# Performance work log

Measured on AMD Instinct MI355X. Metric: run time of the kernel, lower is better.

Reference implementation:

```python
import jax, jax.numpy as jnp
import numpy as np

B, R, N = 1, 1024, 128
C_FEAT, C_MSA, C_PAIR = 22, 256, 128
NBINS = 65  # relpos bins, vbins = arange(65) - 32


def setup_inputs() -> dict:
    key = jax.random.key(0)
    ks = jax.random.split(key, 9)
    w = lambda k, shape: (jax.random.normal(k, shape, jnp.float32) * 0.05)
    return {
        "target_feat": jax.random.normal(ks[0], (B, R, C_FEAT), jnp.float32),
        "residue_index": jnp.broadcast_to(jnp.arange(R, dtype=jnp.int32), (B, R)),
        "msa_feat": jax.random.normal(ks[1], (B, N, R, C_FEAT), jnp.float32),
        "Wa": w(ks[2], (C_PAIR, C_FEAT)), "ba": jnp.zeros((C_PAIR,), jnp.float32),
        "Wb": w(ks[3], (C_PAIR, C_FEAT)), "bb": jnp.zeros((C_PAIR,), jnp.float32),
        "Wm1": w(ks[4], (C_MSA, C_FEAT)), "bm1": jnp.zeros((C_MSA,), jnp.float32),
        "Wm2": w(ks[5], (C_MSA, C_FEAT)), "bm2": jnp.zeros((C_MSA,), jnp.float32),
        "Wpos": w(ks[6], (C_PAIR, NBINS)), "bpos": jnp.zeros((C_PAIR,), jnp.float32),
    }


def reference(target_feat, residue_index, msa_feat,
              Wa, ba, Wb, bb, Wm1, bm1, Wm2, bm2, Wpos, bpos):
    # pair init: z[b,i,j] = to_a(tf)[b,j] + to_b(tf)[b,i]
    a = target_feat @ Wa.T + ba                      # (b, r, c_pair)
    bv = target_feat @ Wb.T + bb                     # (b, r, c_pair)
    z = a[:, None, :, :] + bv[:, :, None, :]         # (b, r, r, c_pair)

    # relpos: nearest-bin one-hot of d = ri[j] - ri[i] against arange(65)-32,
    # then Linear(65 -> c_pair).  One-hot @ W.T is exactly an embedding gather
    # of row clip(d+32, 0, 64) from Wpos.T, so skip materializing the one-hot.
    d = residue_index[:, None, :] - residue_index[:, :, None]  # (b, r, r)
    bins = jnp.clip(d + (NBINS // 2), 0, NBINS - 1)            # (b, r, r) int
    z = z + Wpos.T[bins] + bpos                                # gather + bias

    # MSA init: m = to_m1(msa_feat) + to_m2(target_feat) broadcast over n rows
    m = (msa_feat @ Wm1.T + bm1) + (target_feat @ Wm2.T + bm2)[:, None, :, :]
    return m, z
```

## Files before the change

kernel.cpp:

```cpp
#include <hip/hip_runtime.h>

#define RR     1024
#define NSEQ   128
#define CFEAT  22
#define CMSA   256
#define CPAIR  128
#define NBINS  65

typedef float f4 __attribute__((ext_vector_type(4)));

__global__ __launch_bounds__(256) void k_pre(
    const float* __restrict__ tf,
    const float* __restrict__ Wa, const float* __restrict__ ba,
    const float* __restrict__ Wb, const float* __restrict__ bb,
    const float* __restrict__ Wm2, const float* __restrict__ bm2,
    const float* __restrict__ Wpos, const float* __restrict__ bpos,
    float* __restrict__ a, float* __restrict__ bvp,
    float* __restrict__ tm2, float* __restrict__ pose)
{
    __shared__ float wlds[CFEAT][512];
    __shared__ float row[CFEAT];
    const int r = blockIdx.x;
    const int t = threadIdx.x;

    for (int idx = t; idx < 128 * CFEAT; idx += 256) {
        int c = idx / CFEAT, k = idx - c * CFEAT;
        wlds[k][c] = Wa[idx];
    }
    for (int idx = t; idx < 128 * CFEAT; idx += 256) {
        int c = idx / CFEAT, k = idx - c * CFEAT;
        wlds[k][128 + c] = Wb[idx];
    }
    for (int idx = t; idx < 256 * CFEAT; idx += 256) {
        int c = idx / CFEAT, k = idx - c * CFEAT;
        wlds[k][256 + c] = Wm2[idx];
    }
    if (t < CFEAT) row[t] = tf[r * CFEAT + t];
    __syncthreads();

    float s1 = 0.f, s2 = 0.f;
    #pragma unroll
    for (int k = 0; k < CFEAT; ++k) {
        float rv = row[k];
        s1 += rv * wlds[k][t];
        s2 += rv * wlds[k][256 + t];
    }
    tm2[(long)r * CMSA + t] = s2 + bm2[t];
    if (t < CPAIR) a[(long)r * CPAIR + t] = s1 + ba[t];
    else           bvp[(long)r * CPAIR + (t - CPAIR)] = s1 + bb[t - CPAIR];

    if (r < NBINS && t < CPAIR)
        pose[r * CPAIR + t] = Wpos[t * NBINS + r] + bpos[t];
}

#define PPB 64
__global__ __launch_bounds__(256) void k_msa(
    const float* __restrict__ msa,
    const float* __restrict__ Wm1, const float* __restrict__ bm1,
    const float* __restrict__ tm2, float* __restrict__ out_m)
{
    __shared__ float wt[CFEAT][CMSA];
    __shared__ float rows[PPB][24];
    const int t = threadIdx.x;

    for (int idx = t; idx < CMSA * CFEAT; idx += 256) {
        int c = idx / CFEAT, k = idx - c * CFEAT;
        wt[k][c] = Wm1[idx];
    }
    const long pbase = (long)blockIdx.x * PPB;
    const float* src = msa + pbase * CFEAT;
    for (int idx = t; idx < PPB * CFEAT; idx += 256) {
        int p = idx / CFEAT, k = idx - p * CFEAT;
        rows[p][k] = src[idx];
    }
    if (t < PPB) { rows[t][22] = 0.f; rows[t][23] = 0.f; }
    __syncthreads();

    const int c  = (t & 63) * 4;
    const int wv = t >> 6;

    f4 wr[24];
    #pragma unroll
    for (int k = 0; k < CFEAT; ++k) wr[k] = *(const f4*)&wt[k][c];
    wr[22] = (f4){0.f, 0.f, 0.f, 0.f};
    wr[23] = (f4){0.f, 0.f, 0.f, 0.f};
    const f4 b4 = *(const f4*)(bm1 + c);

    for (int it = 0; it < PPB / 4; ++it) {
        const int p = it * 4 + wv;
        const long pair = pbase + p;
        const int r = (int)(pair & (RR - 1));
        f4 acc = (f4){0.f, 0.f, 0.f, 0.f};
        #pragma unroll
        for (int k4 = 0; k4 < 6; ++k4) {
            f4 mv = *(const f4*)&rows[p][k4 * 4];
            acc += mv.x * wr[k4 * 4 + 0];
            acc += mv.y * wr[k4 * 4 + 1];
            acc += mv.z * wr[k4 * 4 + 2];
            acc += mv.w * wr[k4 * 4 + 3];
        }
        const f4 t4 = *(const f4*)(tm2 + (long)r * CMSA + c);
        f4 o = acc + b4 + t4;
        __builtin_nontemporal_store(o, (f4*)(out_m + pair * CMSA + c));
    }
}

__global__ __launch_bounds__(256) void k_pair(
    const int* __restrict__ resi,
    const float* __restrict__ a, const float* __restrict__ bvp,
    const float* __restrict__ pose, float* __restrict__ out_z)
{
    const int bx = blockIdx.x;
    const int i = bx >> 4;
    const int jbase = (bx & 15) * 64;
    const int t = threadIdx.x;
    const int c4 = (t & 31);
    const int jo = t >> 5;

    const int ri = resi[i];
    const f4 bvv = *(const f4*)(bvp + (long)i * CPAIR + c4 * 4);

    #pragma unroll
    for (int jj = 0; jj < 64; jj += 8) {
        const int j = jbase + jj + jo;
        int d = resi[j] - ri + (NBINS / 2);
        d = min(max(d, 0), NBINS - 1);
        const f4 av = *(const f4*)(a + (long)j * CPAIR + c4 * 4);
        const f4 pv = *(const f4*)(pose + (long)d * CPAIR + c4 * 4);
        f4 o = av + bvv + pv;
        __builtin_nontemporal_store(
            o, (f4*)(out_z + ((long)i * RR + j) * CPAIR + c4 * 4));
    }
}

extern "C" void kernel_launch(void* const* d_in, const int* in_sizes, int n_in,
                              void* d_out, int out_size, void* d_ws, size_t ws_size,
                              hipStream_t stream) {
    const float* tf   = (const float*)d_in[0];
    const int*   resi = (const int*)  d_in[1];
    const float* msa  = (const float*)d_in[2];
    const float* Wa   = (const float*)d_in[3];
    const float* ba   = (const float*)d_in[4];
    const float* Wb   = (const float*)d_in[5];
    const float* bb   = (const float*)d_in[6];
    const float* Wm1  = (const float*)d_in[7];
    const float* bm1  = (const float*)d_in[8];
    const float* Wm2  = (const float*)d_in[9];
    const float* bm2  = (const float*)d_in[10];
    const float* Wpos = (const float*)d_in[11];
    const float* bpos = (const float*)d_in[12];

    float* out_m = (float*)d_out;
    float* out_z = out_m + (long)NSEQ * RR * CMSA;

    float* a    = (float*)d_ws;
    float* bvp  = a   + (long)RR * CPAIR;
    float* tm2  = bvp + (long)RR * CPAIR;
    float* pose = tm2 + (long)RR * CMSA;

    k_pre<<<RR, 256, 0, stream>>>(tf, Wa, ba, Wb, bb, Wm2, bm2, Wpos, bpos,
                                  a, bvp, tm2, pose);
    k_msa<<<(NSEQ * RR) / PPB, 256, 0, stream>>>(msa, Wm1, bm1, tm2, out_m);
    k_pair<<<RR * 16, 256, 0, stream>>>(resi, a, bvp, pose, out_z);
}
```

Before: 161.5 us.

## Batch rows per block in prep kernel and stage pose table in LDS for pair kernel

The prep kernel now handles 8 residues per block, so the LDS weight transpose is amortised over 8 rows instead of redone 1024 times. The pair kernel switches to one block per row i with 512 threads. Each block stages the 65x128 pose table and the residue indices in LDS, so the gather reads LDS instead of global memory. This cuts redundant weight loads and launch overhead, but each pair block pays about 37 KB of LDS staging, which may limit occupancy on what is mainly a store-bound kernel.

```diff
diff --git a/kernel.cpp b/kernel.cpp
--- a/kernel.cpp
+++ b/kernel.cpp
@@ -19,9 +19,9 @@
     float* __restrict__ tm2, float* __restrict__ pose)
 {
     __shared__ float wlds[CFEAT][512];
-    __shared__ float row[CFEAT];
-    const int r = blockIdx.x;
+    __shared__ float rows[8][CFEAT];
     const int t = threadIdx.x;
+    const int r0 = blockIdx.x * 8;
 
     for (int idx = t; idx < 128 * CFEAT; idx += 256) {
         int c = idx / CFEAT, k = idx - c * CFEAT;
@@ -35,22 +35,29 @@
         int c = idx / CFEAT, k = idx - c * CFEAT;
         wlds[k][256 + c] = Wm2[idx];
     }
-    if (t < CFEAT) row[t] = tf[r * CFEAT + t];
+    for (int idx = t; idx < 8 * CFEAT; idx += 256) {
+        int rr = idx / CFEAT, k = idx - rr * CFEAT;
+        rows[rr][k] = tf[(r0 + rr) * CFEAT + k];
+    }
     __syncthreads();
 
-    float s1 = 0.f, s2 = 0.f;
     #pragma unroll
-    for (int k = 0; k < CFEAT; ++k) {
-        float rv = row[k];
-        s1 += rv * wlds[k][t];
-        s2 += rv * wlds[k][256 + t];
+    for (int rr = 0; rr < 8; ++rr) {
+        const int r = r0 + rr;
+        float s1 = 0.f, s2 = 0.f;
+        #pragma unroll
+        for (int k = 0; k < CFEAT; ++k) {
+            float rv = rows[rr][k];
+            s1 += rv * wlds[k][t];
+            s2 += rv * wlds[k][256 + t];
+        }
+        tm2[r * CMSA + t] = s2 + bm2[t];
+        if (t < CPAIR) a[r * CPAIR + t] = s1 + ba[t];
+        else           bvp[r * CPAIR + (t - CPAIR)] = s1 + bb[t - CPAIR];
     }
-    tm2[(long)r * CMSA + t] = s2 + bm2[t];
-    if (t < CPAIR) a[(long)r * CPAIR + t] = s1 + ba[t];
-    else           bvp[(long)r * CPAIR + (t - CPAIR)] = s1 + bb[t - CPAIR];
 
-    if (r < NBINS && t < CPAIR)
-        pose[r * CPAIR + t] = Wpos[t * NBINS + r] + bpos[t];
+    if (blockIdx.x < NBINS && t < CPAIR)
+        pose[blockIdx.x * CPAIR + t] = Wpos[t * NBINS + blockIdx.x] + bpos[t];
 }
 
 #define PPB 64
@@ -105,31 +112,37 @@
     }
 }
 
-__global__ __launch_bounds__(256) void k_pair(
+__global__ __launch_bounds__(512) void k_pair(
     const int* __restrict__ resi,
     const float* __restrict__ a, const float* __restrict__ bvp,
     const float* __restrict__ pose, float* __restrict__ out_z)
 {
-    const int bx = blockIdx.x;
-    const int i = bx >> 4;
-    const int jbase = (bx & 15) * 64;
+    __shared__ float poseL[NBINS][CPAIR];
+    __shared__ int   rjL[RR];
+    const int i = blockIdx.x;
     const int t = threadIdx.x;
-    const int c4 = (t & 31);
+
+    for (int idx = t; idx < NBINS * CPAIR; idx += 512)
+        (&poseL[0][0])[idx] = pose[idx];
+    for (int idx = t; idx < RR; idx += 512)
+        rjL[idx] = resi[idx];
+    __syncthreads();
+
+    const int c4 = (t & 31) * 4;
     const int jo = t >> 5;
+    const int ri = rjL[i];
+    const f4 bvv = *(const f4*)(bvp + (long)i * CPAIR + c4);
+    float* dst = out_z + (long)i * RR * CPAIR;
 
-    const int ri = resi[i];
-    const f4 bvv = *(const f4*)(bvp + (long)i * CPAIR + c4 * 4);
-
-    #pragma unroll
-    for (int jj = 0; jj < 64; jj += 8) {
-        const int j = jbase + jj + jo;
-        int d = resi[j] - ri + (NBINS / 2);
+    #pragma unroll 4
+    for (int jj = 0; jj < RR; jj += 16) {
+        const int j = jj + jo;
+        int d = rjL[j] - ri + (NBINS / 2);
         d = min(max(d, 0), NBINS - 1);
-        const f4 av = *(const f4*)(a + (long)j * CPAIR + c4 * 4);
-        const f4 pv = *(const f4*)(pose + (long)d * CPAIR + c4 * 4);
+        const f4 av = *(const f4*)(a + (long)j * CPAIR + c4);
+        const f4 pv = *(const f4*)&poseL[d][c4];
         f4 o = av + bvv + pv;
-        __builtin_nontemporal_store(
-            o, (f4*)(out_z + ((long)i * RR + j) * CPAIR + c4 * 4));
+        __builtin_nontemporal_store(o, (f4*)(dst + (long)j * CPAIR + c4));
     }
 }
 
@@ -158,8 +171,8 @@
     float* tm2  = bvp + (long)RR * CPAIR;
     float* pose = tm2 + (long)RR * CMSA;
 
-    k_pre<<<RR, 256, 0, stream>>>(tf, Wa, ba, Wb, bb, Wm2, bm2, Wpos, bpos,
-                                  a, bvp, tm2, pose);
+    k_pre<<<128, 256, 0, stream>>>(tf, Wa, ba, Wb, bb, Wm2, bm2, Wpos, bpos,
+                                   a, bvp, tm2, pose);
     k_msa<<<(NSEQ * RR) / PPB, 256, 0, stream>>>(msa, Wm1, bm1, tm2, out_m);
-    k_pair<<<RR * 16, 256, 0, stream>>>(resi, a, bvp, pose, out_z);
+    k_pair<<<RR, 512, 0, stream>>>(resi, a, bvp, pose, out_z);
 }
```

New measurement: 157.2 us. 1.03x faster.
